# Kernel optimization log

Measured on AMD Instinct MI355X. Metric: run time of the kernel, lower is better.

## Reference

```python
import jax, jax.numpy as jnp
import numpy as np
import math

N_NODES = 100000
N_EDGES = 1600000
DIM = 64


def setup_inputs() -> dict:
    key = jax.random.key(0)
    ks = jax.random.split(key, 16)
    s = 1.0 / math.sqrt(DIM)
    inp = {
        "x": jax.random.normal(ks[0], (N_NODES, DIM), jnp.float32),
        "edge_vec": jax.random.normal(ks[1], (N_EDGES, 3), jnp.float32),
        # lin_Q / lin_K / lin_V
        "Wq": jax.random.normal(ks[2], (DIM, DIM), jnp.float32) * s,
        "bq": jnp.zeros((DIM,), jnp.float32),
        "Wk": jax.random.normal(ks[3], (DIM, DIM), jnp.float32) * s,
        "bk": jnp.zeros((DIM,), jnp.float32),
        "Wv": jax.random.normal(ks[4], (DIM, DIM), jnp.float32) * s,
        "bv": jnp.zeros((DIM,), jnp.float32),
        # edge_bias MLP: [4 -> dim -> dim -> 1], SiLU between layers
        "W1": jax.random.normal(ks[5], (4, DIM), jnp.float32) * 0.5,
        "b1": jnp.zeros((DIM,), jnp.float32),
        "W2": jax.random.normal(ks[6], (DIM, DIM), jnp.float32) * s,
        "b2": jnp.zeros((DIM,), jnp.float32),
        "W3": jax.random.normal(ks[7], (DIM, 1), jnp.float32) * s,
        "b3": jnp.zeros((1,), jnp.float32),
        # w_F
        "wF": jax.random.normal(ks[8], (DIM, 1), jnp.float32) * s,
        "bF": jnp.zeros((1,), jnp.float32),
        "edge_index": jax.random.randint(ks[9], (2, N_EDGES), 0, N_NODES, jnp.int32),
    }
    return inp


def reference(x, edge_vec, Wq, bq, Wk, bk, Wv, bv, W1, b1, W2, b2, W3, b3, wF, bF, edge_index):
    n = x.shape[0]
    dim = x.shape[1]
    i = edge_index[0]
    j = edge_index[1]

    # project on nodes (N << E), then gather to edges
    query = (x @ Wq + bq)[j]          # [E, dim]
    key = (x @ Wk + bk)[i]            # [E, dim]
    value = (x @ Wv + bv)[i]          # [E, dim]

    # edge MLP bias on [vec, |vec|]
    edge_len = jnp.linalg.norm(edge_vec, axis=-1, keepdims=True)  # [E, 1]
    edge_attr = jnp.concatenate([edge_vec, edge_len], axis=-1)    # [E, 4]
    h = jax.nn.silu(edge_attr @ W1 + b1)
    h = jax.nn.silu(h @ W2 + b2)
    bias = (h @ W3 + b3)[:, 0]        # [E]

    scores = jnp.sum(query * key, axis=-1) / jnp.sqrt(jnp.asarray(dim, x.dtype)) + bias  # [E]

    # segment softmax over target node j
    smax = jax.ops.segment_max(scores, j, num_segments=n)
    smax = jnp.where(jnp.isfinite(smax), smax, 0.0)
    ex = jnp.exp(scores - smax[j])
    denom = jax.ops.segment_sum(ex, j, num_segments=n)
    alpha = ex / (denom[j] + 1e-16)   # [E]

    # scatter-weighted vector aggregation
    gate = value @ wF + bF            # [E, 1]
    vec_out = jax.ops.segment_sum(alpha[:, None] * gate * edge_vec, j, num_segments=n)  # [N, 3]
    return vec_out
```

## Files before the change

### kernel.cpp

```cpp
#include <hip/hip_runtime.h>
#include <hip/hip_bf16.h>
#include <math.h>

#define DIM 64
#define NP 65
#define NPTS (NP*NP*NP)
#define TBL_SCALE 5.8181818f
#define TBL_STEP 0.171875f

typedef __attribute__((ext_vector_type(8))) short bf16x8;
typedef __attribute__((ext_vector_type(4))) float f32x4;
typedef __attribute__((ext_vector_type(2))) float f32x2;
typedef unsigned short ushort_t;

__device__ __forceinline__ float silu_f(float x) {
    float e = __expf(-x);
    return x * __builtin_amdgcn_rcpf(1.0f + e);
}
__device__ __forceinline__ unsigned short f2bf_fast(float x) {
    unsigned u = __builtin_bit_cast(unsigned, x);
    u += 0x7FFFu + ((u >> 16) & 1u);
    return (unsigned short)(u >> 16);
}
__device__ __forceinline__ unsigned cvtpk_bf16(float a, float b) {
    unsigned r;
    asm("v_cvt_pk_bf16_f32 %0, %1, %2" : "=v"(r) : "v"(a), "v"(b));
    return r;
}
__device__ __forceinline__ f32x2 pk_fma2(f32x2 a, f32x2 b, f32x2 c) {
    f32x2 d;
    asm("v_pk_fma_f32 %0, %1, %2, %3" : "=v"(d) : "v"(a), "v"(b), "v"(c));
    return d;
}
__device__ __forceinline__ f32x2 pk_add2(f32x2 a, f32x2 b) {
    f32x2 d;
    asm("v_pk_add_f32 %0, %1, %2" : "=v"(d) : "v"(a), "v"(b));
    return d;
}
__device__ __forceinline__ f32x2 bc2(float x) { f32x2 r; r.x = x; r.y = x; return r; }
__device__ __forceinline__ float swz_add(float v, const int pat) {
    int iv = __builtin_bit_cast(int, v);
    int sv;
    switch (pat) {
        case 1: sv = __builtin_amdgcn_ds_swizzle(iv, 0x041F); break;
        case 2: sv = __builtin_amdgcn_ds_swizzle(iv, 0x081F); break;
        case 4: sv = __builtin_amdgcn_ds_swizzle(iv, 0x101F); break;
        default: sv = __builtin_amdgcn_ds_swizzle(iv, 0x201F); break;
    }
    return v + __builtin_bit_cast(float, sv);
}

__global__ __launch_bounds__(256) void k_proj_mfma(
    const float* __restrict__ x,
    const float* __restrict__ Wq, const float* __restrict__ bq,
    const float* __restrict__ Wk, const float* __restrict__ bk,
    const float* __restrict__ Wv, const float* __restrict__ bv,
    const float* __restrict__ wF, const float* __restrict__ bF,
    ushort_t* __restrict__ Qh, ushort_t* __restrict__ Kh,
    float* __restrict__ gate, float* __restrict__ out4,
    int nNodes, int nTiles)
{
    __shared__ float sU[64];
    __shared__ float sC0;

    const int tid = threadIdx.x;
    const int lane = tid & 63;
    const int w = tid >> 6;
    const int lanen = lane & 15;
    const int q = lane >> 4;

    if (tid < 64) {
        const float4* wvr = (const float4*)(Wv + (size_t)lane * 64);
        float accu = 0.f;
        #pragma unroll
        for (int n4 = 0; n4 < 16; ++n4) {
            float4 wv = wvr[n4];
            accu = fmaf(wv.x, wF[n4 * 4 + 0], accu);
            accu = fmaf(wv.y, wF[n4 * 4 + 1], accu);
            accu = fmaf(wv.z, wF[n4 * 4 + 2], accu);
            accu = fmaf(wv.w, wF[n4 * 4 + 3], accu);
        }
        sU[lane] = accu;
        float pc = bv[lane] * wF[lane];
        #pragma unroll
        for (int off = 32; off; off >>= 1) pc += __shfl_xor(pc, off, 64);
        if (lane == 0) sC0 = pc + bF[0];
    }

    bf16x8 Bq[2][4], Bk[2][4];
    #pragma unroll
    for (int c = 0; c < 2; ++c)
        #pragma unroll
        for (int t = 0; t < 4; ++t) {
            bf16x8 vq, vk;
            #pragma unroll
            for (int j = 0; j < 8; ++j) {
                int idx = (c * 32 + q * 8 + j) * 64 + t * 16 + lanen;
                vq[j] = (short)f2bf_fast(Wq[idx]);
                vk[j] = (short)f2bf_fast(Wk[idx]);
            }
            Bq[c][t] = vq; Bk[c][t] = vk;
        }
    const float4* bq4p = (const float4*)bq;
    const float4* bk4p = (const float4*)bk;
    float4 bq4[4], bk4[4];
    #pragma unroll
    for (int t = 0; t < 4; ++t) { bq4[t] = bq4p[t * 4 + q]; bk4[t] = bk4p[t * 4 + q]; }

    __syncthreads();
    const float c0 = sC0;
    float ur0[8], ur1[8];
    #pragma unroll
    for (int j = 0; j < 8; ++j) { ur0[j] = sU[q * 8 + j]; ur1[j] = sU[32 + q * 8 + j]; }

    const int waveId = blockIdx.x * 4 + w;
    const int wstride = gridDim.x * 4;

    for (int tile = waveId; tile < nTiles; tile += wstride) {
        int node0 = tile * 16;
        int nodeA = node0 + lanen;
        int nodeC = (nodeA < nNodes) ? nodeA : (nNodes - 1);
        const float4* xr = (const float4*)(x + (size_t)nodeC * 64);
        float4 xa = xr[q * 2], xb = xr[q * 2 + 1];
        float4 xc = xr[8 + q * 2], xd = xr[8 + q * 2 + 1];

        float g = xa.x * ur0[0] + xa.y * ur0[1] + xa.z * ur0[2] + xa.w * ur0[3]
                + xb.x * ur0[4] + xb.y * ur0[5] + xb.z * ur0[6] + xb.w * ur0[7]
                + xc.x * ur1[0] + xc.y * ur1[1] + xc.z * ur1[2] + xc.w * ur1[3]
                + xd.x * ur1[4] + xd.y * ur1[5] + xd.z * ur1[6] + xd.w * ur1[7];
        g += __shfl_xor(g, 16);
        g += __shfl_xor(g, 32);

        bf16x8 a0, a1;
        a0[0] = (short)f2bf_fast(xa.x); a0[1] = (short)f2bf_fast(xa.y);
        a0[2] = (short)f2bf_fast(xa.z); a0[3] = (short)f2bf_fast(xa.w);
        a0[4] = (short)f2bf_fast(xb.x); a0[5] = (short)f2bf_fast(xb.y);
        a0[6] = (short)f2bf_fast(xb.z); a0[7] = (short)f2bf_fast(xb.w);
        a1[0] = (short)f2bf_fast(xc.x); a1[1] = (short)f2bf_fast(xc.y);
        a1[2] = (short)f2bf_fast(xc.z); a1[3] = (short)f2bf_fast(xc.w);
        a1[4] = (short)f2bf_fast(xd.x); a1[5] = (short)f2bf_fast(xd.y);
        a1[6] = (short)f2bf_fast(xd.z); a1[7] = (short)f2bf_fast(xd.w);

        f32x4 accq[4] = {{0,0,0,0},{0,0,0,0},{0,0,0,0},{0,0,0,0}};
        f32x4 acck[4] = {{0,0,0,0},{0,0,0,0},{0,0,0,0},{0,0,0,0}};
        __builtin_amdgcn_s_setprio(1);
        #pragma unroll
        for (int t = 0; t < 4; ++t) {
            accq[t] = __builtin_amdgcn_mfma_f32_16x16x32_bf16(Bq[0][t], a0, accq[t], 0, 0, 0);
            accq[t] = __builtin_amdgcn_mfma_f32_16x16x32_bf16(Bq[1][t], a1, accq[t], 0, 0, 0);
            acck[t] = __builtin_amdgcn_mfma_f32_16x16x32_bf16(Bk[0][t], a0, acck[t], 0, 0, 0);
            acck[t] = __builtin_amdgcn_mfma_f32_16x16x32_bf16(Bk[1][t], a1, acck[t], 0, 0, 0);
        }
        __builtin_amdgcn_s_setprio(0);

        if (nodeA < nNodes) {
            ushort_t* qrow = Qh + (size_t)nodeA * 64 + q * 4;
            ushort_t* krow = Kh + (size_t)nodeA * 64 + q * 4;
            #pragma unroll
            for (int t = 0; t < 4; ++t) {
                f32x2 q01 = pk_add2((f32x2){accq[t][0], accq[t][1]}, (f32x2){bq4[t].x, bq4[t].y});
                f32x2 q23 = pk_add2((f32x2){accq[t][2], accq[t][3]}, (f32x2){bq4[t].z, bq4[t].w});
                uint2 pq;
                pq.x = cvtpk_bf16(q01.x, q01.y);
                pq.y = cvtpk_bf16(q23.x, q23.y);
                *(uint2*)(qrow + t * 16) = pq;
                f32x2 k01 = pk_add2((f32x2){acck[t][0], acck[t][1]}, (f32x2){bk4[t].x, bk4[t].y});
                f32x2 k23 = pk_add2((f32x2){acck[t][2], acck[t][3]}, (f32x2){bk4[t].z, bk4[t].w});
                uint2 pk;
                pk.x = cvtpk_bf16(k01.x, k01.y);
                pk.y = cvtpk_bf16(k23.x, k23.y);
                *(uint2*)(krow + t * 16) = pk;
            }
            if (q == 0) gate[nodeA] = g + c0;
            if (q == 1) *(float4*)(out4 + (size_t)nodeA * 4) = make_float4(0.f, 0.f, 0.f, 0.f);
        }
    }
}

__global__ __launch_bounds__(256) void k_table(
    const float* __restrict__ W1, const float* __restrict__ b1,
    const float* __restrict__ W2, const float* __restrict__ b2,
    const float* __restrict__ W3, const float* __restrict__ b3,
    float* __restrict__ table)
{
    __shared__ __align__(16) float4 sW1x[72];
    __shared__ __align__(8) f32x2 sB1p[32];

    const int tid = threadIdx.x;
    const int lane = tid & 63;
    const int lanen = lane & 15;
    const int q = lane >> 4;
    const int w = tid >> 6;

    if (tid < 64) {
        int pp = tid >> 1, hh = tid & 1;
        int d0 = pp * 2, k0 = hh * 2;
        sW1x[tid + (tid >> 3)] = make_float4(
            W1[k0 * 64 + d0], W1[k0 * 64 + d0 + 1],
            W1[(k0 + 1) * 64 + d0], W1[(k0 + 1) * 64 + d0 + 1]);
    }
    if (tid < 32) {
        f32x2 bp; bp.x = b1[2 * tid]; bp.y = b1[2 * tid + 1];
        sB1p[tid] = bp;
    }

    bf16x8 Bfrag[2][4];
    #pragma unroll
    for (int c = 0; c < 2; ++c)
        #pragma unroll
        for (int t = 0; t < 4; ++t) {
            bf16x8 v;
            #pragma unroll
            for (int j = 0; j < 8; ++j)
                v[j] = (short)f2bf_fast(W2[(c * 32 + q * 8 + j) * 64 + t * 16 + lanen]);
            Bfrag[c][t] = v;
        }
    float w3r[4];
    f32x2 b2p[4];
    #pragma unroll
    for (int t = 0; t < 4; ++t) {
        b2p[t] = bc2(b2[t * 16 + lanen]);
        w3r[t] = W3[t * 16 + lanen];
    }
    const float b3r = b3[0];
    const int rsel = lanen & 3;
    const int bperm_addr = ((((lanen >> 2) << 4) | lanen) << 2);
    const int slotA0 = q * 9;
    const int slotB0 = 36 + q * 9;
    __syncthreads();

    const int nTilesT = (NPTS + 15) / 16;
    const int wstride = gridDim.x * 4;

    for (int tile = blockIdx.x * 4 + w; tile < nTilesT; tile += wstride) {
        int id = tile * 16 + lanen;
        int idc = (id < NPTS) ? id : (NPTS - 1);
        int iz = idc % NP; int rem = idc / NP;
        int iy = rem % NP; int ix = rem / NP;
        float ax = fmaf((float)ix, TBL_STEP, -5.5f);
        float ay = fmaf((float)iy, TBL_STEP, -5.5f);
        float az = fmaf((float)iz, TBL_STEP, -5.5f);
        float4 attr = make_float4(ax, ay, az, sqrtf(ax * ax + ay * ay + az * az));

        f32x2 ax2 = bc2(attr.x), ay2 = bc2(attr.y), az2 = bc2(attr.z), aw2 = bc2(attr.w);
        int pw0[4], pw1[4];
        #pragma unroll
        for (int s = 0; s < 4; ++s) {
            float4 wa0 = sW1x[slotA0 + 2 * s];
            float4 wa1 = sW1x[slotA0 + 2 * s + 1];
            f32x2 hA = sB1p[q * 4 + s];
            hA = pk_fma2((f32x2){wa0.x, wa0.y}, ax2, hA);
            hA = pk_fma2((f32x2){wa0.z, wa0.w}, ay2, hA);
            hA = pk_fma2((f32x2){wa1.x, wa1.y}, az2, hA);
            hA = pk_fma2((f32x2){wa1.z, wa1.w}, aw2, hA);
            float4 wb0 = sW1x[slotB0 + 2 * s];
            float4 wb1 = sW1x[slotB0 + 2 * s + 1];
            f32x2 hB = sB1p[16 + q * 4 + s];
            hB = pk_fma2((f32x2){wb0.x, wb0.y}, ax2, hB);
            hB = pk_fma2((f32x2){wb0.z, wb0.w}, ay2, hB);
            hB = pk_fma2((f32x2){wb1.x, wb1.y}, az2, hB);
            hB = pk_fma2((f32x2){wb1.z, wb1.w}, aw2, hB);
            pw0[s] = (int)cvtpk_bf16(silu_f(hA.x), silu_f(hA.y));
            pw1[s] = (int)cvtpk_bf16(silu_f(hB.x), silu_f(hB.y));
        }
        bf16x8 a0 = __builtin_bit_cast(bf16x8, make_int4(pw0[0], pw0[1], pw0[2], pw0[3]));
        bf16x8 a1 = __builtin_bit_cast(bf16x8, make_int4(pw1[0], pw1[1], pw1[2], pw1[3]));

        f32x4 acc[4] = {{0,0,0,0},{0,0,0,0},{0,0,0,0},{0,0,0,0}};
        #pragma unroll
        for (int t = 0; t < 4; ++t) {
            acc[t] = __builtin_amdgcn_mfma_f32_16x16x32_bf16(a0, Bfrag[0][t], acc[t], 0, 0, 0);
            acc[t] = __builtin_amdgcn_mfma_f32_16x16x32_bf16(a1, Bfrag[1][t], acc[t], 0, 0, 0);
        }

        float part[4] = {0.f, 0.f, 0.f, 0.f};
        #pragma unroll
        for (int t = 0; t < 4; ++t) {
            f32x2 s01 = pk_add2((f32x2){acc[t][0], acc[t][1]}, b2p[t]);
            f32x2 s23 = pk_add2((f32x2){acc[t][2], acc[t][3]}, b2p[t]);
            part[0] = fmaf(silu_f(s01.x), w3r[t], part[0]);
            part[1] = fmaf(silu_f(s01.y), w3r[t], part[1]);
            part[2] = fmaf(silu_f(s23.x), w3r[t], part[2]);
            part[3] = fmaf(silu_f(s23.y), w3r[t], part[3]);
        }
        #pragma unroll
        for (int r = 0; r < 4; ++r) {
            part[r] = swz_add(part[r], 1);
            part[r] = swz_add(part[r], 2);
            part[r] = swz_add(part[r], 4);
            part[r] = swz_add(part[r], 8);
        }

        float psel = part[0];
        psel = (rsel == 1) ? part[1] : psel;
        psel = (rsel == 2) ? part[2] : psel;
        psel = (rsel == 3) ? part[3] : psel;
        int moved = __builtin_amdgcn_ds_bpermute(bperm_addr, __builtin_bit_cast(int, psel));
        float bias = __builtin_bit_cast(float, moved) + b3r;

        if (q == 0 && id < NPTS) table[id] = bias;
    }
}

__global__ __launch_bounds__(256) void k_edge_mfma(
    const int* __restrict__ ei, const int* __restrict__ ej,
    const ushort_t* __restrict__ Qh, const ushort_t* __restrict__ Kh,
    const float* __restrict__ gate, const float* __restrict__ edge_vec,
    const float* __restrict__ table,
    float* __restrict__ out4, int nEdges, long nTiles)
{
    const int tid = threadIdx.x;
    const int lane = tid & 63;
    const int lanen = lane & 15;
    const int q = lane >> 4;
    const int w = tid >> 6;
    const int rsel = lanen & 3;
    const int bperm_addr = ((((lanen >> 2) << 4) | lanen) << 2);

    const long wstride = (long)gridDim.x * 4;
    const long t0 = (long)blockIdx.x * 4 + w;

    auto idx_of = [&](long tile, int& ii, int& jj) {
        long es = tile * 16 + lanen;
        long esc = (es < nEdges) ? es : (long)(nEdges - 1);
        ii = ei[esc]; jj = ej[esc];
    };
    auto gather = [&](long tile, int ii, int jj,
                      bf16x8& A, bf16x8& B, bf16x8& C, bf16x8& D, float& G,
                      float& ax, float& ay, float& az,
                      float& fx, float& fy, float& fz,
                      float& c000, float& c001, float& c010, float& c011,
                      float& c100, float& c101, float& c110, float& c111) {
        const bf16x8* qp = (const bf16x8*)(Qh + (size_t)jj * 64);
        A = qp[q]; B = qp[4 + q];
        const bf16x8* kp = (const bf16x8*)(Kh + (size_t)ii * 64);
        C = kp[q]; D = kp[4 + q];
        G = gate[ii];
        long em = tile * 16 + lanen;
        long emc = (em < nEdges) ? em : (long)(nEdges - 1);
        ax = edge_vec[emc * 3 + 0];
        ay = edge_vec[emc * 3 + 1];
        az = edge_vec[emc * 3 + 2];
        float tx = fminf(fmaxf(fmaf(ax, TBL_SCALE, 32.0f), 0.0f), 63.999f);
        float ty = fminf(fmaxf(fmaf(ay, TBL_SCALE, 32.0f), 0.0f), 63.999f);
        float tz = fminf(fmaxf(fmaf(az, TBL_SCALE, 32.0f), 0.0f), 63.999f);
        int ix = (int)tx, iy = (int)ty, iz = (int)tz;
        fx = tx - (float)ix; fy = ty - (float)iy; fz = tz - (float)iz;
        const float* T0 = table + ((ix * NP + iy) * NP + iz);
        const float* T1 = T0 + NP * NP;
        c000 = T0[0];      c001 = T0[1];
        c010 = T0[NP];     c011 = T0[NP + 1];
        c100 = T1[0];      c101 = T1[1];
        c110 = T1[NP];     c111 = T1[NP + 1];
    };

    int iC, jC, iN, jN;
    idx_of(t0, iC, jC);
    idx_of(t0 + wstride, iN, jN);
    bf16x8 qa = {}, qb = {}, ka = {}, kb = {};
    float gte = 0.f, vax = 0.f, vay = 0.f, vaz = 0.f;
    float fx = 0.f, fy = 0.f, fz = 0.f;
    float c000 = 0.f, c001 = 0.f, c010 = 0.f, c011 = 0.f;
    float c100 = 0.f, c101 = 0.f, c110 = 0.f, c111 = 0.f;
    gather(t0, iC, jC, qa, qb, ka, kb, gte, vax, vay, vaz, fx, fy, fz,
           c000, c001, c010, c011, c100, c101, c110, c111);

    for (long tile = t0; tile < nTiles; tile += wstride) {
        __builtin_amdgcn_s_setprio(1);
        f32x4 accd = {0.f, 0.f, 0.f, 0.f};
        accd = __builtin_amdgcn_mfma_f32_16x16x32_bf16(qa, ka, accd, 0, 0, 0);
        accd = __builtin_amdgcn_mfma_f32_16x16x32_bf16(qb, kb, accd, 0, 0, 0);
        __builtin_amdgcn_s_setprio(0);

        int iF, jF;
        idx_of(tile + 2 * wstride, iF, jF);
        bf16x8 qa2 = {}, qb2 = {}, ka2 = {}, kb2 = {};
        float gte2 = 0.f, vax2 = 0.f, vay2 = 0.f, vaz2 = 0.f;
        float fx2 = 0.f, fy2 = 0.f, fz2 = 0.f;
        float d000 = 0.f, d001 = 0.f, d010 = 0.f, d011 = 0.f;
        float d100 = 0.f, d101 = 0.f, d110 = 0.f, d111 = 0.f;
        gather(tile + wstride, iN, jN, qa2, qb2, ka2, kb2, gte2, vax2, vay2, vaz2,
               fx2, fy2, fz2, d000, d001, d010, d011, d100, d101, d110, d111);

        float a00 = fmaf(fz, c001 - c000, c000);
        float a01 = fmaf(fz, c011 - c010, c010);
        float a10 = fmaf(fz, c101 - c100, c100);
        float a11 = fmaf(fz, c111 - c110, c110);
        float b0 = fmaf(fy, a01 - a00, a00);
        float b1 = fmaf(fy, a11 - a10, a10);
        float bias = fmaf(fx, b1 - b0, b0);

        float dsel = accd[0];
        dsel = (rsel == 1) ? accd[1] : dsel;
        dsel = (rsel == 2) ? accd[2] : dsel;
        dsel = (rsel == 3) ? accd[3] : dsel;
        int moved = __builtin_amdgcn_ds_bpermute(bperm_addr, __builtin_bit_cast(int, dsel));
        float sc = fmaf(__builtin_bit_cast(float, moved), 0.125f, bias);

        float ev = __expf(sc);
        long eC = tile * 16 + lanen;
        if (eC < nEdges) {
            float comp = (q == 0) ? vax : (q == 1) ? vay : vaz;
            float vout = (q == 3) ? ev : ev * gte * comp;
            atomicAdd(out4 + (size_t)jC * 4 + q, vout);
        }

        iC = iN; jC = jN; iN = iF; jN = jF;
        qa = qa2; qb = qb2; ka = ka2; kb = kb2;
        gte = gte2; vax = vax2; vay = vay2; vaz = vaz2;
        fx = fx2; fy = fy2; fz = fz2;
        c000 = d000; c001 = d001; c010 = d010; c011 = d011;
        c100 = d100; c101 = d101; c110 = d110; c111 = d111;
    }
}

__global__ __launch_bounds__(256) void k_div(
    const float4* __restrict__ out4, float* __restrict__ out, int nNodes)
{
    int j = blockIdx.x * 256 + threadIdx.x;
    if (j >= nNodes) return;
    float4 v = out4[j];
    float inv = 1.0f / (v.w + 1e-16f);
    out[(size_t)j * 3 + 0] = v.x * inv;
    out[(size_t)j * 3 + 1] = v.y * inv;
    out[(size_t)j * 3 + 2] = v.z * inv;
}

extern "C" void kernel_launch(void* const* d_in, const int* in_sizes, int n_in,
                              void* d_out, int out_size, void* d_ws, size_t ws_size,
                              hipStream_t stream)
{
    const float* x        = (const float*)d_in[0];
    const float* edge_vec = (const float*)d_in[1];
    const float* Wq = (const float*)d_in[2];
    const float* bq = (const float*)d_in[3];
    const float* Wk = (const float*)d_in[4];
    const float* bk = (const float*)d_in[5];
    const float* Wv = (const float*)d_in[6];
    const float* bv = (const float*)d_in[7];
    const float* W1 = (const float*)d_in[8];
    const float* b1 = (const float*)d_in[9];
    const float* W2 = (const float*)d_in[10];
    const float* b2 = (const float*)d_in[11];
    const float* W3 = (const float*)d_in[12];
    const float* b3 = (const float*)d_in[13];
    const float* wF = (const float*)d_in[14];
    const float* bF = (const float*)d_in[15];
    const int*   eidx = (const int*)d_in[16];

    int nNodes = in_sizes[0] / DIM;
    int nEdges = in_sizes[16] / 2;
    const int* ei = eidx;
    const int* ej = eidx + nEdges;

    char* p = (char*)d_ws;
    ushort_t* Qh = (ushort_t*)p;
    ushort_t* Kh = Qh + (size_t)nNodes * DIM;
    p += (size_t)nNodes * DIM * 2 * sizeof(ushort_t);
    float* gate = (float*)p;   p += (size_t)nNodes * sizeof(float);
    float* out4 = (float*)p;   p += (size_t)nNodes * 4 * sizeof(float);
    float* table = (float*)p;  p += (size_t)NPTS * sizeof(float);

    float* out = (float*)d_out;

    int nTilesN = (nNodes + 15) / 16;
    k_proj_mfma<<<1024, 256, 0, stream>>>(x, Wq, bq, Wk, bk, Wv, bv, wF, bF,
                                          Qh, Kh, gate, out4, nNodes, nTilesN);

    k_table<<<1024, 256, 0, stream>>>(W1, b1, W2, b2, W3, b3, table);

    long nTilesE = (nEdges + 15) / 16;
    k_edge_mfma<<<2048, 256, 0, stream>>>(ei, ej, Qh, Kh, gate, edge_vec, table,
                                          out4, nEdges, nTilesE);

    int nBn = (nNodes + 255) / 256;
    k_div<<<nBn, 256, 0, stream>>>((const float4*)out4, out, nNodes);
}
```

Measured before the change: 248.8 us.

## Fuse projection and table kernels; store bias table as float4 corners; planar accumulators

The node-projection and bias-table kernels merge into one launch, with block ranges split between the two jobs so they run concurrently and one launch is saved. The bias table now stores four neighbouring z/y corners per cell as a float4, so each edge fetches its eight trilinear corners with two 16-byte loads instead of eight scattered scalar loads. Output accumulators change from interleaved float4-per-node to four separate planes, so each quarter-wave's atomics target one contiguous plane. In exchange, the table is four times larger and table construction does extra redundant stores.

```diff
diff --git a/kernel.cpp b/kernel.cpp
--- a/kernel.cpp
+++ b/kernel.cpp
@@ -7,6 +7,8 @@
 #define NPTS (NP*NP*NP)
 #define TBL_SCALE 5.8181818f
 #define TBL_STEP 0.171875f
+#define PROJ_BLOCKS 1024
+#define TAB_BLOCKS 512
 
 typedef __attribute__((ext_vector_type(8))) short bf16x8;
 typedef __attribute__((ext_vector_type(4))) float f32x4;
@@ -50,18 +52,24 @@
     return v + __builtin_bit_cast(float, sv);
 }
 
-__global__ __launch_bounds__(256) void k_proj_mfma(
+__global__ __launch_bounds__(256) void k_proj_tab(
     const float* __restrict__ x,
     const float* __restrict__ Wq, const float* __restrict__ bq,
     const float* __restrict__ Wk, const float* __restrict__ bk,
     const float* __restrict__ Wv, const float* __restrict__ bv,
     const float* __restrict__ wF, const float* __restrict__ bF,
+    const float* __restrict__ W1, const float* __restrict__ b1,
+    const float* __restrict__ W2, const float* __restrict__ b2,
+    const float* __restrict__ W3, const float* __restrict__ b3,
     ushort_t* __restrict__ Qh, ushort_t* __restrict__ Kh,
-    float* __restrict__ gate, float* __restrict__ out4,
+    float* __restrict__ gate, float* __restrict__ outP, int strideP,
+    float* __restrict__ table4v,
     int nNodes, int nTiles)
 {
     __shared__ float sU[64];
     __shared__ float sC0;
+    __shared__ __align__(16) float4 sW1x[72];
+    __shared__ __align__(8) f32x2 sB1p[32];
 
     const int tid = threadIdx.x;
     const int lane = tid & 63;
@@ -69,236 +77,228 @@
     const int lanen = lane & 15;
     const int q = lane >> 4;
 
-    if (tid < 64) {
-        const float4* wvr = (const float4*)(Wv + (size_t)lane * 64);
-        float accu = 0.f;
+    if (blockIdx.x < PROJ_BLOCKS) {
+        if (tid < 64) {
+            const float4* wvr = (const float4*)(Wv + (size_t)lane * 64);
+            float accu = 0.f;
+            #pragma unroll
+            for (int n4 = 0; n4 < 16; ++n4) {
+                float4 wv = wvr[n4];
+                accu = fmaf(wv.x, wF[n4 * 4 + 0], accu);
+                accu = fmaf(wv.y, wF[n4 * 4 + 1], accu);
+                accu = fmaf(wv.z, wF[n4 * 4 + 2], accu);
+                accu = fmaf(wv.w, wF[n4 * 4 + 3], accu);
+            }
+            sU[lane] = accu;
+            float pc = bv[lane] * wF[lane];
+            #pragma unroll
+            for (int off = 32; off; off >>= 1) pc += __shfl_xor(pc, off, 64);
+            if (lane == 0) sC0 = pc + bF[0];
+        }
+
+        bf16x8 Bq[2][4], Bk[2][4];
         #pragma unroll
-        for (int n4 = 0; n4 < 16; ++n4) {
-            float4 wv = wvr[n4];
-            accu = fmaf(wv.x, wF[n4 * 4 + 0], accu);
-            accu = fmaf(wv.y, wF[n4 * 4 + 1], accu);
-            accu = fmaf(wv.z, wF[n4 * 4 + 2], accu);
-            accu = fmaf(wv.w, wF[n4 * 4 + 3], accu);
-        }
-        sU[lane] = accu;
-        float pc = bv[lane] * wF[lane];
+        for (int c = 0; c < 2; ++c)
+            #pragma unroll
+            for (int t = 0; t < 4; ++t) {
+                bf16x8 vq, vk;
+                #pragma unroll
+                for (int j = 0; j < 8; ++j) {
+                    int idx = (c * 32 + q * 8 + j) * 64 + t * 16 + lanen;
+                    vq[j] = (short)f2bf_fast(Wq[idx]);
+                    vk[j] = (short)f2bf_fast(Wk[idx]);
+                }
+                Bq[c][t] = vq; Bk[c][t] = vk;
+            }
+        const float4* bq4p = (const float4*)bq;
+        const float4* bk4p = (const float4*)bk;
+        float4 bq4[4], bk4[4];
         #pragma unroll
-        for (int off = 32; off; off >>= 1) pc += __shfl_xor(pc, off, 64);
-        if (lane == 0) sC0 = pc + bF[0];
-    }
-
-    bf16x8 Bq[2][4], Bk[2][4];
-    #pragma unroll
-    for (int c = 0; c < 2; ++c)
+        for (int t = 0; t < 4; ++t) { bq4[t] = bq4p[t * 4 + q]; bk4[t] = bk4p[t * 4 + q]; }
+
+        __syncthreads();
+        const float c0 = sC0;
+        float ur0[8], ur1[8];
+        #pragma unroll
+        for (int j = 0; j < 8; ++j) { ur0[j] = sU[q * 8 + j]; ur1[j] = sU[32 + q * 8 + j]; }
+
+        const int waveId = blockIdx.x * 4 + w;
+        const int wstride = PROJ_BLOCKS * 4;
+
+        for (int tile = waveId; tile < nTiles; tile += wstride) {
+            int node0 = tile * 16;
+            int nodeA = node0 + lanen;
+            int nodeC = (nodeA < nNodes) ? nodeA : (nNodes - 1);
+            const float4* xr = (const float4*)(x + (size_t)nodeC * 64);
+            float4 xa = xr[q * 2], xb = xr[q * 2 + 1];
+            float4 xc = xr[8 + q * 2], xd = xr[8 + q * 2 + 1];
+
+            float g = xa.x * ur0[0] + xa.y * ur0[1] + xa.z * ur0[2] + xa.w * ur0[3]
+                    + xb.x * ur0[4] + xb.y * ur0[5] + xb.z * ur0[6] + xb.w * ur0[7]
+                    + xc.x * ur1[0] + xc.y * ur1[1] + xc.z * ur1[2] + xc.w * ur1[3]
+                    + xd.x * ur1[4] + xd.y * ur1[5] + xd.z * ur1[6] + xd.w * ur1[7];
+            g += __shfl_xor(g, 16);
+            g += __shfl_xor(g, 32);
+
+            bf16x8 a0, a1;
+            a0[0] = (short)f2bf_fast(xa.x); a0[1] = (short)f2bf_fast(xa.y);
+            a0[2] = (short)f2bf_fast(xa.z); a0[3] = (short)f2bf_fast(xa.w);
+            a0[4] = (short)f2bf_fast(xb.x); a0[5] = (short)f2bf_fast(xb.y);
+            a0[6] = (short)f2bf_fast(xb.z); a0[7] = (short)f2bf_fast(xb.w);
+            a1[0] = (short)f2bf_fast(xc.x); a1[1] = (short)f2bf_fast(xc.y);
+            a1[2] = (short)f2bf_fast(xc.z); a1[3] = (short)f2bf_fast(xc.w);
+            a1[4] = (short)f2bf_fast(xd.x); a1[5] = (short)f2bf_fast(xd.y);
+            a1[6] = (short)f2bf_fast(xd.z); a1[7] = (short)f2bf_fast(xd.w);
+
+            f32x4 accq[4] = {{0,0,0,0},{0,0,0,0},{0,0,0,0},{0,0,0,0}};
+            f32x4 acck[4] = {{0,0,0,0},{0,0,0,0},{0,0,0,0},{0,0,0,0}};
+            __builtin_amdgcn_s_setprio(1);
+            #pragma unroll
+            for (int t = 0; t < 4; ++t) {
+                accq[t] = __builtin_amdgcn_mfma_f32_16x16x32_bf16(Bq[0][t], a0, accq[t], 0, 0, 0);
+                accq[t] = __builtin_amdgcn_mfma_f32_16x16x32_bf16(Bq[1][t], a1, accq[t], 0, 0, 0);
+                acck[t] = __builtin_amdgcn_mfma_f32_16x16x32_bf16(Bk[0][t], a0, acck[t], 0, 0, 0);
+                acck[t] = __builtin_amdgcn_mfma_f32_16x16x32_bf16(Bk[1][t], a1, acck[t], 0, 0, 0);
+            }
+            __builtin_amdgcn_s_setprio(0);
+
+            if (nodeA < nNodes) {
+                ushort_t* qrow = Qh + (size_t)nodeA * 64 + q * 4;
+                ushort_t* krow = Kh + (size_t)nodeA * 64 + q * 4;
+                #pragma unroll
+                for (int t = 0; t < 4; ++t) {
+                    f32x2 q01 = pk_add2((f32x2){accq[t][0], accq[t][1]}, (f32x2){bq4[t].x, bq4[t].y});
+                    f32x2 q23 = pk_add2((f32x2){accq[t][2], accq[t][3]}, (f32x2){bq4[t].z, bq4[t].w});
+                    uint2 pq;
+                    pq.x = cvtpk_bf16(q01.x, q01.y);
+                    pq.y = cvtpk_bf16(q23.x, q23.y);
+                    *(uint2*)(qrow + t * 16) = pq;
+                    f32x2 k01 = pk_add2((f32x2){acck[t][0], acck[t][1]}, (f32x2){bk4[t].x, bk4[t].y});
+                    f32x2 k23 = pk_add2((f32x2){acck[t][2], acck[t][3]}, (f32x2){bk4[t].z, bk4[t].w});
+                    uint2 pk;
+                    pk.x = cvtpk_bf16(k01.x, k01.y);
+                    pk.y = cvtpk_bf16(k23.x, k23.y);
+                    *(uint2*)(krow + t * 16) = pk;
+                }
+                if (q == 0) gate[nodeA] = g + c0;
+                outP[(size_t)q * strideP + nodeA] = 0.f;
+            }
+        }
+    } else {
+        if (tid < 64) {
+            int pp = tid >> 1, hh = tid & 1;
+            int d0 = pp * 2, k0 = hh * 2;
+            sW1x[tid + (tid >> 3)] = make_float4(
+                W1[k0 * 64 + d0], W1[k0 * 64 + d0 + 1],
+                W1[(k0 + 1) * 64 + d0], W1[(k0 + 1) * 64 + d0 + 1]);
+        }
+        if (tid < 32) {
+            f32x2 bp; bp.x = b1[2 * tid]; bp.y = b1[2 * tid + 1];
+            sB1p[tid] = bp;
+        }
+
+        bf16x8 Bfrag[2][4];
+        #pragma unroll
+        for (int c = 0; c < 2; ++c)
+            #pragma unroll
+            for (int t = 0; t < 4; ++t) {
+                bf16x8 v;
+                #pragma unroll
+                for (int j = 0; j < 8; ++j)
+                    v[j] = (short)f2bf_fast(W2[(c * 32 + q * 8 + j) * 64 + t * 16 + lanen]);
+                Bfrag[c][t] = v;
+            }
+        float w3r[4];
+        f32x2 b2p[4];
         #pragma unroll
         for (int t = 0; t < 4; ++t) {
-            bf16x8 vq, vk;
-            #pragma unroll
-            for (int j = 0; j < 8; ++j) {
-                int idx = (c * 32 + q * 8 + j) * 64 + t * 16 + lanen;
-                vq[j] = (short)f2bf_fast(Wq[idx]);
-                vk[j] = (short)f2bf_fast(Wk[idx]);
-            }
-            Bq[c][t] = vq; Bk[c][t] = vk;
-        }
-    const float4* bq4p = (const float4*)bq;
-    const float4* bk4p = (const float4*)bk;
-    float4 bq4[4], bk4[4];
-    #pragma unroll
-    for (int t = 0; t < 4; ++t) { bq4[t] = bq4p[t * 4 + q]; bk4[t] = bk4p[t * 4 + q]; }
-
-    __syncthreads();
-    const float c0 = sC0;
-    float ur0[8], ur1[8];
-    #pragma unroll
-    for (int j = 0; j < 8; ++j) { ur0[j] = sU[q * 8 + j]; ur1[j] = sU[32 + q * 8 + j]; }
-
-    const int waveId = blockIdx.x * 4 + w;
-    const int wstride = gridDim.x * 4;
-
-    for (int tile = waveId; tile < nTiles; tile += wstride) {
-        int node0 = tile * 16;
-        int nodeA = node0 + lanen;
-        int nodeC = (nodeA < nNodes) ? nodeA : (nNodes - 1);
-        const float4* xr = (const float4*)(x + (size_t)nodeC * 64);
-        float4 xa = xr[q * 2], xb = xr[q * 2 + 1];
-        float4 xc = xr[8 + q * 2], xd = xr[8 + q * 2 + 1];
-
-        float g = xa.x * ur0[0] + xa.y * ur0[1] + xa.z * ur0[2] + xa.w * ur0[3]
-                + xb.x * ur0[4] + xb.y * ur0[5] + xb.z * ur0[6] + xb.w * ur0[7]
-                + xc.x * ur1[0] + xc.y * ur1[1] + xc.z * ur1[2] + xc.w * ur1[3]
-                + xd.x * ur1[4] + xd.y * ur1[5] + xd.z * ur1[6] + xd.w * ur1[7];
-        g += __shfl_xor(g, 16);
-        g += __shfl_xor(g, 32);
-
-        bf16x8 a0, a1;
-        a0[0] = (short)f2bf_fast(xa.x); a0[1] = (short)f2bf_fast(xa.y);
-        a0[2] = (short)f2bf_fast(xa.z); a0[3] = (short)f2bf_fast(xa.w);
-        a0[4] = (short)f2bf_fast(xb.x); a0[5] = (short)f2bf_fast(xb.y);
-        a0[6] = (short)f2bf_fast(xb.z); a0[7] = (short)f2bf_fast(xb.w);
-        a1[0] = (short)f2bf_fast(xc.x); a1[1] = (short)f2bf_fast(xc.y);
-        a1[2] = (short)f2bf_fast(xc.z); a1[3] = (short)f2bf_fast(xc.w);
-        a1[4] = (short)f2bf_fast(xd.x); a1[5] = (short)f2bf_fast(xd.y);
-        a1[6] = (short)f2bf_fast(xd.z); a1[7] = (short)f2bf_fast(xd.w);
-
-        f32x4 accq[4] = {{0,0,0,0},{0,0,0,0},{0,0,0,0},{0,0,0,0}};
-        f32x4 acck[4] = {{0,0,0,0},{0,0,0,0},{0,0,0,0},{0,0,0,0}};
-        __builtin_amdgcn_s_setprio(1);
-        #pragma unroll
-        for (int t = 0; t < 4; ++t) {
-            accq[t] = __builtin_amdgcn_mfma_f32_16x16x32_bf16(Bq[0][t], a0, accq[t], 0, 0, 0);
-            accq[t] = __builtin_amdgcn_mfma_f32_16x16x32_bf16(Bq[1][t], a1, accq[t], 0, 0, 0);
-            acck[t] = __builtin_amdgcn_mfma_f32_16x16x32_bf16(Bk[0][t], a0, acck[t], 0, 0, 0);
-            acck[t] = __builtin_amdgcn_mfma_f32_16x16x32_bf16(Bk[1][t], a1, acck[t], 0, 0, 0);
-        }
-        __builtin_amdgcn_s_setprio(0);
-
-        if (nodeA < nNodes) {
-            ushort_t* qrow = Qh + (size_t)nodeA * 64 + q * 4;
-            ushort_t* krow = Kh + (size_t)nodeA * 64 + q * 4;
+            b2p[t] = bc2(b2[t * 16 + lanen]);
+            w3r[t] = W3[t * 16 + lanen];
+        }
+        const float b3r = b3[0];
+        const int rsel = lanen & 3;
+        const int bperm_addr = ((((lanen >> 2) << 4) | lanen) << 2);
+        const int slotA0 = q * 9;
+        const int slotB0 = 36 + q * 9;
+        __syncthreads();
+
+        const int nTilesT = (NPTS + 15) / 16;
+        const int wstride = TAB_BLOCKS * 4;
+
+        for (int tile = (blockIdx.x - PROJ_BLOCKS) * 4 + w; tile < nTilesT; tile += wstride) {
+            int id = tile * 16 + lanen;
+            int idc = (id < NPTS) ? id : (NPTS - 1);
+            int iz = idc % NP; int rem = idc / NP;
+            int iy = rem % NP; int ix = rem / NP;
+            float ax = fmaf((float)ix, TBL_STEP, -5.5f);
+            float ay = fmaf((float)iy, TBL_STEP, -5.5f);
+            float az = fmaf((float)iz, TBL_STEP, -5.5f);
+            float4 attr = make_float4(ax, ay, az, sqrtf(ax * ax + ay * ay + az * az));
+
+            f32x2 ax2 = bc2(attr.x), ay2 = bc2(attr.y), az2 = bc2(attr.z), aw2 = bc2(attr.w);
+            int pw0[4], pw1[4];
+            #pragma unroll
+            for (int s = 0; s < 4; ++s) {
+                float4 wa0 = sW1x[slotA0 + 2 * s];
+                float4 wa1 = sW1x[slotA0 + 2 * s + 1];
+                f32x2 hA = sB1p[q * 4 + s];
+                hA = pk_fma2((f32x2){wa0.x, wa0.y}, ax2, hA);
+                hA = pk_fma2((f32x2){wa0.z, wa0.w}, ay2, hA);
+                hA = pk_fma2((f32x2){wa1.x, wa1.y}, az2, hA);
+                hA = pk_fma2((f32x2){wa1.z, wa1.w}, aw2, hA);
+                float4 wb0 = sW1x[slotB0 + 2 * s];
+                float4 wb1 = sW1x[slotB0 + 2 * s + 1];
+                f32x2 hB = sB1p[16 + q * 4 + s];
+                hB = pk_fma2((f32x2){wb0.x, wb0.y}, ax2, hB);
+                hB = pk_fma2((f32x2){wb0.z, wb0.w}, ay2, hB);
+                hB = pk_fma2((f32x2){wb1.x, wb1.y}, az2, hB);
+                hB = pk_fma2((f32x2){wb1.z, wb1.w}, aw2, hB);
+                pw0[s] = (int)cvtpk_bf16(silu_f(hA.x), silu_f(hA.y));
+                pw1[s] = (int)cvtpk_bf16(silu_f(hB.x), silu_f(hB.y));
+            }
+            bf16x8 a0 = __builtin_bit_cast(bf16x8, make_int4(pw0[0], pw0[1], pw0[2], pw0[3]));
+            bf16x8 a1 = __builtin_bit_cast(bf16x8, make_int4(pw1[0], pw1[1], pw1[2], pw1[3]));
+
+            f32x4 acc[4] = {{0,0,0,0},{0,0,0,0},{0,0,0,0},{0,0,0,0}};
             #pragma unroll
             for (int t = 0; t < 4; ++t) {
-                f32x2 q01 = pk_add2((f32x2){accq[t][0], accq[t][1]}, (f32x2){bq4[t].x, bq4[t].y});
-                f32x2 q23 = pk_add2((f32x2){accq[t][2], accq[t][3]}, (f32x2){bq4[t].z, bq4[t].w});
-                uint2 pq;
-                pq.x = cvtpk_bf16(q01.x, q01.y);
-                pq.y = cvtpk_bf16(q23.x, q23.y);
-                *(uint2*)(qrow + t * 16) = pq;
-                f32x2 k01 = pk_add2((f32x2){acck[t][0], acck[t][1]}, (f32x2){bk4[t].x, bk4[t].y});
-                f32x2 k23 = pk_add2((f32x2){acck[t][2], acck[t][3]}, (f32x2){bk4[t].z, bk4[t].w});
-                uint2 pk;
-                pk.x = cvtpk_bf16(k01.x, k01.y);
-                pk.y = cvtpk_bf16(k23.x, k23.y);
-                *(uint2*)(krow + t * 16) = pk;
-            }
-            if (q == 0) gate[nodeA] = g + c0;
-            if (q == 1) *(float4*)(out4 + (size_t)nodeA * 4) = make_float4(0.f, 0.f, 0.f, 0.f);
-        }
-    }
-}
-
-__global__ __launch_bounds__(256) void k_table(
-    const float* __restrict__ W1, const float* __restrict__ b1,
-    const float* __restrict__ W2, const float* __restrict__ b2,
-    const float* __restrict__ W3, const float* __restrict__ b3,
-    float* __restrict__ table)
-{
-    __shared__ __align__(16) float4 sW1x[72];
-    __shared__ __align__(8) f32x2 sB1p[32];
-
-    const int tid = threadIdx.x;
-    const int lane = tid & 63;
-    const int lanen = lane & 15;
-    const int q = lane >> 4;
-    const int w = tid >> 6;
-
-    if (tid < 64) {
-        int pp = tid >> 1, hh = tid & 1;
-        int d0 = pp * 2, k0 = hh * 2;
-        sW1x[tid + (tid >> 3)] = make_float4(
-            W1[k0 * 64 + d0], W1[k0 * 64 + d0 + 1],
-            W1[(k0 + 1) * 64 + d0], W1[(k0 + 1) * 64 + d0 + 1]);
-    }
-    if (tid < 32) {
-        f32x2 bp; bp.x = b1[2 * tid]; bp.y = b1[2 * tid + 1];
-        sB1p[tid] = bp;
-    }
-
-    bf16x8 Bfrag[2][4];
-    #pragma unroll
-    for (int c = 0; c < 2; ++c)
-        #pragma unroll
-        for (int t = 0; t < 4; ++t) {
-            bf16x8 v;
-            #pragma unroll
-            for (int j = 0; j < 8; ++j)
-                v[j] = (short)f2bf_fast(W2[(c * 32 + q * 8 + j) * 64 + t * 16 + lanen]);
-            Bfrag[c][t] = v;
-        }
-    float w3r[4];
-    f32x2 b2p[4];
-    #pragma unroll
-    for (int t = 0; t < 4; ++t) {
-        b2p[t] = bc2(b2[t * 16 + lanen]);
-        w3r[t] = W3[t * 16 + lanen];
-    }
-    const float b3r = b3[0];
-    const int rsel = lanen & 3;
-    const int bperm_addr = ((((lanen >> 2) << 4) | lanen) << 2);
-    const int slotA0 = q * 9;
-    const int slotB0 = 36 + q * 9;
-    __syncthreads();
-
-    const int nTilesT = (NPTS + 15) / 16;
-    const int wstride = gridDim.x * 4;
-
-    for (int tile = blockIdx.x * 4 + w; tile < nTilesT; tile += wstride) {
-        int id = tile * 16 + lanen;
-        int idc = (id < NPTS) ? id : (NPTS - 1);
-        int iz = idc % NP; int rem = idc / NP;
-        int iy = rem % NP; int ix = rem / NP;
-        float ax = fmaf((float)ix, TBL_STEP, -5.5f);
-        float ay = fmaf((float)iy, TBL_STEP, -5.5f);
-        float az = fmaf((float)iz, TBL_STEP, -5.5f);
-        float4 attr = make_float4(ax, ay, az, sqrtf(ax * ax + ay * ay + az * az));
-
-        f32x2 ax2 = bc2(attr.x), ay2 = bc2(attr.y), az2 = bc2(attr.z), aw2 = bc2(attr.w);
-        int pw0[4], pw1[4];
-        #pragma unroll
-        for (int s = 0; s < 4; ++s) {
-            float4 wa0 = sW1x[slotA0 + 2 * s];
-            float4 wa1 = sW1x[slotA0 + 2 * s + 1];
-            f32x2 hA = sB1p[q * 4 + s];
-            hA = pk_fma2((f32x2){wa0.x, wa0.y}, ax2, hA);
-            hA = pk_fma2((f32x2){wa0.z, wa0.w}, ay2, hA);
-            hA = pk_fma2((f32x2){wa1.x, wa1.y}, az2, hA);
-            hA = pk_fma2((f32x2){wa1.z, wa1.w}, aw2, hA);
-            float4 wb0 = sW1x[slotB0 + 2 * s];
-            float4 wb1 = sW1x[slotB0 + 2 * s + 1];
-            f32x2 hB = sB1p[16 + q * 4 + s];
-            hB = pk_fma2((f32x2){wb0.x, wb0.y}, ax2, hB);
-            hB = pk_fma2((f32x2){wb0.z, wb0.w}, ay2, hB);
-            hB = pk_fma2((f32x2){wb1.x, wb1.y}, az2, hB);
-            hB = pk_fma2((f32x2){wb1.z, wb1.w}, aw2, hB);
-            pw0[s] = (int)cvtpk_bf16(silu_f(hA.x), silu_f(hA.y));
-            pw1[s] = (int)cvtpk_bf16(silu_f(hB.x), silu_f(hB.y));
-        }
-        bf16x8 a0 = __builtin_bit_cast(bf16x8, make_int4(pw0[0], pw0[1], pw0[2], pw0[3]));
-        bf16x8 a1 = __builtin_bit_cast(bf16x8, make_int4(pw1[0], pw1[1], pw1[2], pw1[3]));
-
-        f32x4 acc[4] = {{0,0,0,0},{0,0,0,0},{0,0,0,0},{0,0,0,0}};
-        #pragma unroll
-        for (int t = 0; t < 4; ++t) {
-            acc[t] = __builtin_amdgcn_mfma_f32_16x16x32_bf16(a0, Bfrag[0][t], acc[t], 0, 0, 0);
-            acc[t] = __builtin_amdgcn_mfma_f32_16x16x32_bf16(a1, Bfrag[1][t], acc[t], 0, 0, 0);
-        }
-
-        float part[4] = {0.f, 0.f, 0.f, 0.f};
-        #pragma unroll
-        for (int t = 0; t < 4; ++t) {
-            f32x2 s01 = pk_add2((f32x2){acc[t][0], acc[t][1]}, b2p[t]);
-            f32x2 s23 = pk_add2((f32x2){acc[t][2], acc[t][3]}, b2p[t]);
-            part[0] = fmaf(silu_f(s01.x), w3r[t], part[0]);
-            part[1] = fmaf(silu_f(s01.y), w3r[t], part[1]);
-            part[2] = fmaf(silu_f(s23.x), w3r[t], part[2]);
-            part[3] = fmaf(silu_f(s23.y), w3r[t], part[3]);
-        }
-        #pragma unroll
-        for (int r = 0; r < 4; ++r) {
-            part[r] = swz_add(part[r], 1);
-            part[r] = swz_add(part[r], 2);
-            part[r] = swz_add(part[r], 4);
-            part[r] = swz_add(part[r], 8);
-        }
-
-        float psel = part[0];
-        psel = (rsel == 1) ? part[1] : psel;
-        psel = (rsel == 2) ? part[2] : psel;
-        psel = (rsel == 3) ? part[3] : psel;
-        int moved = __builtin_amdgcn_ds_bpermute(bperm_addr, __builtin_bit_cast(int, psel));
-        float bias = __builtin_bit_cast(float, moved) + b3r;
-
-        if (q == 0 && id < NPTS) table[id] = bias;
+                acc[t] = __builtin_amdgcn_mfma_f32_16x16x32_bf16(a0, Bfrag[0][t], acc[t], 0, 0, 0);
+                acc[t] = __builtin_amdgcn_mfma_f32_16x16x32_bf16(a1, Bfrag[1][t], acc[t], 0, 0, 0);
+            }
+
+            float part[4] = {0.f, 0.f, 0.f, 0.f};
+            #pragma unroll
+            for (int t = 0; t < 4; ++t) {
+                f32x2 s01 = pk_add2((f32x2){acc[t][0], acc[t][1]}, b2p[t]);
+                f32x2 s23 = pk_add2((f32x2){acc[t][2], acc[t][3]}, b2p[t]);
+                part[0] = fmaf(silu_f(s01.x), w3r[t], part[0]);
+                part[1] = fmaf(silu_f(s01.y), w3r[t], part[1]);
+                part[2] = fmaf(silu_f(s23.x), w3r[t], part[2]);
+                part[3] = fmaf(silu_f(s23.y), w3r[t], part[3]);
+            }
+            #pragma unroll
+            for (int r = 0; r < 4; ++r) {
+                part[r] = swz_add(part[r], 1);
+                part[r] = swz_add(part[r], 2);
+                part[r] = swz_add(part[r], 4);
+                part[r] = swz_add(part[r], 8);
+            }
+
+            float psel = part[0];
+            psel = (rsel == 1) ? part[1] : psel;
+            psel = (rsel == 2) ? part[2] : psel;
+            psel = (rsel == 3) ? part[3] : psel;
+            int moved = __builtin_amdgcn_ds_bpermute(bperm_addr, __builtin_bit_cast(int, psel));
+            float bias = __builtin_bit_cast(float, moved) + b3r;
+
+            if (q == 0 && id < NPTS) {
+                int base = idc;
+                table4v[(size_t)base * 4 + 0] = bias;
+                if (iz > 0) table4v[(size_t)(base - 1) * 4 + 1] = bias;
+                if (iy > 0) table4v[(size_t)(base - NP) * 4 + 2] = bias;
+                if (iy > 0 && iz > 0) table4v[(size_t)(base - NP - 1) * 4 + 3] = bias;
+            }
+        }
     }
 }
 
@@ -306,8 +306,8 @@
     const int* __restrict__ ei, const int* __restrict__ ej,
     const ushort_t* __restrict__ Qh, const ushort_t* __restrict__ Kh,
     const float* __restrict__ gate, const float* __restrict__ edge_vec,
-    const float* __restrict__ table,
-    float* __restrict__ out4, int nEdges, long nTiles)
+    const float4* __restrict__ table4,
+    float* __restrict__ outP, int strideP, int nEdges, long nTiles)
 {
     const int tid = threadIdx.x;
     const int lane = tid & 63;
@@ -319,6 +319,7 @@
 
     const long wstride = (long)gridDim.x * 4;
     const long t0 = (long)blockIdx.x * 4 + w;
+    float* const planeQ = outP + (size_t)q * strideP;
 
     auto idx_of = [&](long tile, int& ii, int& jj) {
         long es = tile * 16 + lanen;
@@ -329,8 +330,7 @@
                       bf16x8& A, bf16x8& B, bf16x8& C, bf16x8& D, float& G,
                       float& ax, float& ay, float& az,
                       float& fx, float& fy, float& fz,
-                      float& c000, float& c001, float& c010, float& c011,
-                      float& c100, float& c101, float& c110, float& c111) {
+                      float4& TA, float4& TB) {
         const bf16x8* qp = (const bf16x8*)(Qh + (size_t)jj * 64);
         A = qp[q]; B = qp[4 + q];
         const bf16x8* kp = (const bf16x8*)(Kh + (size_t)ii * 64);
@@ -346,12 +346,9 @@
         float tz = fminf(fmaxf(fmaf(az, TBL_SCALE, 32.0f), 0.0f), 63.999f);
         int ix = (int)tx, iy = (int)ty, iz = (int)tz;
         fx = tx - (float)ix; fy = ty - (float)iy; fz = tz - (float)iz;
-        const float* T0 = table + ((ix * NP + iy) * NP + iz);
-        const float* T1 = T0 + NP * NP;
-        c000 = T0[0];      c001 = T0[1];
-        c010 = T0[NP];     c011 = T0[NP + 1];
-        c100 = T1[0];      c101 = T1[1];
-        c110 = T1[NP];     c111 = T1[NP + 1];
+        int cell = (ix * NP + iy) * NP + iz;
+        TA = table4[cell];
+        TB = table4[cell + NP * NP];
     };
 
     int iC, jC, iN, jN;
@@ -360,10 +357,9 @@
     bf16x8 qa = {}, qb = {}, ka = {}, kb = {};
     float gte = 0.f, vax = 0.f, vay = 0.f, vaz = 0.f;
     float fx = 0.f, fy = 0.f, fz = 0.f;
-    float c000 = 0.f, c001 = 0.f, c010 = 0.f, c011 = 0.f;
-    float c100 = 0.f, c101 = 0.f, c110 = 0.f, c111 = 0.f;
-    gather(t0, iC, jC, qa, qb, ka, kb, gte, vax, vay, vaz, fx, fy, fz,
-           c000, c001, c010, c011, c100, c101, c110, c111);
+    float4 tA = make_float4(0.f, 0.f, 0.f, 0.f);
+    float4 tB = make_float4(0.f, 0.f, 0.f, 0.f);
+    gather(t0, iC, jC, qa, qb, ka, kb, gte, vax, vay, vaz, fx, fy, fz, tA, tB);
 
     for (long tile = t0; tile < nTiles; tile += wstride) {
         __builtin_amdgcn_s_setprio(1);
@@ -377,17 +373,17 @@
         bf16x8 qa2 = {}, qb2 = {}, ka2 = {}, kb2 = {};
         float gte2 = 0.f, vax2 = 0.f, vay2 = 0.f, vaz2 = 0.f;
         float fx2 = 0.f, fy2 = 0.f, fz2 = 0.f;
-        float d000 = 0.f, d001 = 0.f, d010 = 0.f, d011 = 0.f;
-        float d100 = 0.f, d101 = 0.f, d110 = 0.f, d111 = 0.f;
+        float4 tA2 = make_float4(0.f, 0.f, 0.f, 0.f);
+        float4 tB2 = make_float4(0.f, 0.f, 0.f, 0.f);
         gather(tile + wstride, iN, jN, qa2, qb2, ka2, kb2, gte2, vax2, vay2, vaz2,
-               fx2, fy2, fz2, d000, d001, d010, d011, d100, d101, d110, d111);
-
-        float a00 = fmaf(fz, c001 - c000, c000);
-        float a01 = fmaf(fz, c011 - c010, c010);
-        float a10 = fmaf(fz, c101 - c100, c100);
-        float a11 = fmaf(fz, c111 - c110, c110);
-        float b0 = fmaf(fy, a01 - a00, a00);
-        float b1 = fmaf(fy, a11 - a10, a10);
+               fx2, fy2, fz2, tA2, tB2);
+
+        float a00 = fmaf(fz, tA.y - tA.x, tA.x);
+        float a01 = fmaf(fz, tA.w - tA.z, tA.z);
+        float b0  = fmaf(fy, a01 - a00, a00);
+        float a10 = fmaf(fz, tB.y - tB.x, tB.x);
+        float a11 = fmaf(fz, tB.w - tB.z, tB.z);
+        float b1  = fmaf(fy, a11 - a10, a10);
         float bias = fmaf(fx, b1 - b0, b0);
 
         float dsel = accd[0];
@@ -402,28 +398,31 @@
         if (eC < nEdges) {
             float comp = (q == 0) ? vax : (q == 1) ? vay : vaz;
             float vout = (q == 3) ? ev : ev * gte * comp;
-            atomicAdd(out4 + (size_t)jC * 4 + q, vout);
+            atomicAdd(planeQ + jC, vout);
         }
 
         iC = iN; jC = jN; iN = iF; jN = jF;
         qa = qa2; qb = qb2; ka = ka2; kb = kb2;
         gte = gte2; vax = vax2; vay = vay2; vaz = vaz2;
         fx = fx2; fy = fy2; fz = fz2;
-        c000 = d000; c001 = d001; c010 = d010; c011 = d011;
-        c100 = d100; c101 = d101; c110 = d110; c111 = d111;
+        tA = tA2; tB = tB2;
     }
 }
 
 __global__ __launch_bounds__(256) void k_div(
-    const float4* __restrict__ out4, float* __restrict__ out, int nNodes)
+    const float* __restrict__ outP, int strideP,
+    float* __restrict__ out, int nNodes)
 {
     int j = blockIdx.x * 256 + threadIdx.x;
     if (j >= nNodes) return;
-    float4 v = out4[j];
-    float inv = 1.0f / (v.w + 1e-16f);
-    out[(size_t)j * 3 + 0] = v.x * inv;
-    out[(size_t)j * 3 + 1] = v.y * inv;
-    out[(size_t)j * 3 + 2] = v.z * inv;
+    float nx = outP[j];
+    float ny = outP[(size_t)strideP + j];
+    float nz = outP[(size_t)2 * strideP + j];
+    float den = outP[(size_t)3 * strideP + j];
+    float inv = 1.0f / (den + 1e-16f);
+    out[(size_t)j * 3 + 0] = nx * inv;
+    out[(size_t)j * 3 + 1] = ny * inv;
+    out[(size_t)j * 3 + 2] = nz * inv;
 }
 
 extern "C" void kernel_launch(void* const* d_in, const int* in_sizes, int n_in,
@@ -452,27 +451,29 @@
     int nEdges = in_sizes[16] / 2;
     const int* ei = eidx;
     const int* ej = eidx + nEdges;
+    int strideP = (nNodes + 63) & ~63;
 
     char* p = (char*)d_ws;
     ushort_t* Qh = (ushort_t*)p;
     ushort_t* Kh = Qh + (size_t)nNodes * DIM;
     p += (size_t)nNodes * DIM * 2 * sizeof(ushort_t);
-    float* gate = (float*)p;   p += (size_t)nNodes * sizeof(float);
-    float* out4 = (float*)p;   p += (size_t)nNodes * 4 * sizeof(float);
-    float* table = (float*)p;  p += (size_t)NPTS * sizeof(float);
+    float* gate = (float*)p;    p += (size_t)nNodes * sizeof(float);
+    float* outP = (float*)p;    p += (size_t)strideP * 4 * sizeof(float);
+    float* table4 = (float*)p;  p += (size_t)NPTS * 4 * sizeof(float);
 
     float* out = (float*)d_out;
 
     int nTilesN = (nNodes + 15) / 16;
-    k_proj_mfma<<<1024, 256, 0, stream>>>(x, Wq, bq, Wk, bk, Wv, bv, wF, bF,
-                                          Qh, Kh, gate, out4, nNodes, nTilesN);
-
-    k_table<<<1024, 256, 0, stream>>>(W1, b1, W2, b2, W3, b3, table);
+    k_proj_tab<<<PROJ_BLOCKS + TAB_BLOCKS, 256, 0, stream>>>(
+        x, Wq, bq, Wk, bk, Wv, bv, wF, bF,
+        W1, b1, W2, b2, W3, b3,
+        Qh, Kh, gate, outP, strideP, table4, nNodes, nTilesN);
 
     long nTilesE = (nEdges + 15) / 16;
-    k_edge_mfma<<<2048, 256, 0, stream>>>(ei, ej, Qh, Kh, gate, edge_vec, table,
-                                          out4, nEdges, nTilesE);
+    k_edge_mfma<<<2048, 256, 0, stream>>>(ei, ej, Qh, Kh, gate, edge_vec,
+                                          (const float4*)table4,
+                                          outP, strideP, nEdges, nTilesE);
 
     int nBn = (nNodes + 255) / 256;
-    k_div<<<nBn, 256, 0, stream>>>((const float4*)out4, out, nNodes);
-}
+    k_div<<<nBn, 256, 0, stream>>>(outP, strideP, out, nNodes);
+}
```

Measured after the change: 465.3 us. 87.0% more time.
